# Optimization experiments

Measured on AMD Instinct MI355X. Metric: run time of the kernel, lower is better.

## Reference

```python
import jax, jax.numpy as jnp
import numpy as np
import math

M = 8                      # multiplicity (channels per irrep)
COMBOS = [(0,0,0),(0,1,1),(1,0,1),(1,1,0),(1,1,1),(2,1,1)]  # (edge_l, node_l, out_l)

def _cg_coeff(j1, m1, j2, m2, j3, m3):
    # standard (Racah) complex Clebsch-Gordan coefficient <j1 m1 j2 m2 | j3 m3>
    if m3 != m1 + m2:
        return 0.0
    f = math.factorial
    vmin = max(0, j2 - j3 - m1, j1 + m2 - j3)
    vmax = min(j1 + j2 - j3, j1 - m1, j2 + m2)
    pref = (2*j3 + 1) * f(j3+j1-j2) * f(j3-j1+j2) * f(j1+j2-j3) / f(j1+j2+j3+1)
    pref *= f(j3+m3) * f(j3-m3) * f(j1-m1) * f(j1+m1) * f(j2-m2) * f(j2+m2)
    s = 0.0
    for v in range(vmin, vmax + 1):
        s += (-1)**v / (f(v) * f(j1+j2-j3-v) * f(j1-m1-v) * f(j2+m2-v)
                        * f(j3-j2+m1+v) * f(j3-j1-m2+v))
    return math.sqrt(pref) * s

def _su2_cg(l1, l2, l3):
    C = np.zeros((2*l1+1, 2*l2+1, 2*l3+1), dtype=np.complex128)
    for m1 in range(-l1, l1+1):
        for m2 in range(-l2, l2+1):
            m3 = m1 + m2
            if -l3 <= m3 <= l3:
                C[m1+l1, m2+l2, m3+l3] = _cg_coeff(l1, m1, l2, m2, l3, m3)
    return C

def _qmat(l):
    # real -> complex spherical-harmonic change of basis (e3nn convention)
    q = np.zeros((2*l+1, 2*l+1), dtype=np.complex128)
    for m in range(-l, 0):
        q[l+m, l+abs(m)] = 1/np.sqrt(2)
        q[l+m, l-abs(m)] = -1j/np.sqrt(2)
    q[l, l] = 1.0
    for m in range(1, l+1):
        q[l+m, l+abs(m)] = (-1)**m / np.sqrt(2)
        q[l+m, l-abs(m)] = 1j * (-1)**m / np.sqrt(2)
    return (-1j)**l * q

def _so3_cg(l1, l2, l3):
    # real-basis CG, normalized to unit Frobenius norm (matches e3nn _so3_clebsch_gordan)
    C = np.einsum('ij,kl,mn,ikn->jlm', _qmat(l1), _qmat(l2),
                  np.conj(_qmat(l3)).T, _su2_cg(l1, l2, l3))
    assert np.abs(C.imag).max() < 1e-6
    C = C.real
    return C / np.linalg.norm(C)

CG = {c: jnp.asarray(_so3_cg(*c), dtype=jnp.float32) for c in COMBOS}


def setup_inputs() -> dict:
    N, E = 100000, 1600000
    ks = jax.random.split(jax.random.key(0), 6)
    return {
        'node_irreps': jax.random.normal(ks[0], (N, 4*M), jnp.float32),
        'edge_index': jax.random.randint(ks[1], (2, E), 0, N, dtype=jnp.int32),
        'sh0': jax.random.normal(ks[2], (E, 1), jnp.float32),
        'sh1': jax.random.normal(ks[3], (E, 3), jnp.float32),
        'sh2': jax.random.normal(ks[4], (E, 5), jnp.float32),
        'W': jax.random.normal(ks[5], (len(COMBOS), M, M), jnp.float32),
    }


def reference(node_irreps, edge_index, sh0, sh1, sh2, W):
    N, E = node_irreps.shape[0], edge_index.shape[1]
    src = node_irreps[edge_index[0]]                    # gather: [E, 4M]
    feats = {0: src[:, :M][:, :, None],                 # scalar channels [E, M, 1]
             1: src[:, M:].reshape(E, M, 3)}            # vector channels [E, M, 3]
    sh = {0: sh0, 1: sh1, 2: sh2}
    msg = {0: jnp.zeros((E, M, 1), node_irreps.dtype),
           1: jnp.zeros((E, M, 3), node_irreps.dtype)}
    for idx, (le, ln, lo) in enumerate(COMBOS):
        # per-edge CG tensor product: [de,dn,do] x [E,de] x [E,M,dn] -> [E,M,do]
        base = jnp.einsum('ijk,ei,emj->emk', CG[(le, ln, lo)], sh[le], feats[ln])
        # channel-mixing scalar weights (in_channel -> out_channel)
        msg[lo] = msg[lo] + jnp.einsum('io,eik->eok', W[idx], base)
    tgt = edge_index[1]
    agg0 = jax.ops.segment_sum(msg[0].reshape(E, M), tgt, num_segments=N)     # [N, M]
    agg1 = jax.ops.segment_sum(msg[1].reshape(E, 3*M), tgt, num_segments=N)   # [N, 3M]
    return jnp.concatenate([agg0, agg1], axis=1)
```

## Files before the change

### kernel.cpp

```cpp
#include <hip/hip_runtime.h>

#define THREADS 256

typedef float v4f __attribute__((ext_vector_type(4)));


__global__ __launch_bounds__(THREADS) void k_hist2(const int* __restrict__ tgt,
                                                   int* __restrict__ cnt,
                                                   int* __restrict__ ke, int E) {
    int e = blockIdx.x * THREADS + threadIdx.x;
    if (e < E) ke[e] = atomicAdd(&cnt[tgt[e]], 1);
}

__global__ __launch_bounds__(THREADS) void k_hist(const int* __restrict__ tgt,
                                                  int* __restrict__ cnt, int E) {
    int e = blockIdx.x * THREADS + threadIdx.x;
    if (e < E) atomicAdd(&cnt[tgt[e]], 1);
}

__global__ __launch_bounds__(THREADS) void k_scan_partial(const int* __restrict__ cnt,
                                                          int* __restrict__ bsum, int N) {
    __shared__ int lds[THREADS];
    int base = blockIdx.x * 1024 + threadIdx.x * 4;
    int s = 0;
    #pragma unroll
    for (int k = 0; k < 4; ++k) { int i = base + k; if (i < N) s += cnt[i]; }
    lds[threadIdx.x] = s; __syncthreads();
    for (int off = THREADS / 2; off > 0; off >>= 1) {
        if (threadIdx.x < off) lds[threadIdx.x] += lds[threadIdx.x + off];
        __syncthreads();
    }
    if (threadIdx.x == 0) bsum[blockIdx.x] = lds[0];
}

__global__ __launch_bounds__(THREADS) void k_scan_final2(int* __restrict__ cnt,
                                                         const int* __restrict__ bsum,
                                                         int* __restrict__ rowptr,
                                                         int N, int E, int NB) {
    __shared__ int lbs[THREADS];
    __shared__ int lds[THREADS];
    const int t = threadIdx.x;

    lbs[t] = (t < NB) ? bsum[t] : 0;
    __syncthreads();
    for (int off = 1; off < THREADS; off <<= 1) {
        int x = (t >= off) ? lbs[t - off] : 0;
        __syncthreads();
        lbs[t] += x;
        __syncthreads();
    }
    const int chunkBase = (blockIdx.x > 0) ? lbs[blockIdx.x - 1] : 0;

    int base = blockIdx.x * 1024 + t * 4;
    int v[4]; int local = 0;
    #pragma unroll
    for (int k = 0; k < 4; ++k) {
        int i = base + k;
        v[k] = (i < N) ? cnt[i] : 0;
        local += v[k];
    }
    lds[t] = local; __syncthreads();
    for (int off = 1; off < THREADS; off <<= 1) {
        int x = (t >= off) ? lds[t - off] : 0;
        __syncthreads();
        lds[t] += x;
        __syncthreads();
    }
    int p = lds[t] - local + chunkBase;
    #pragma unroll
    for (int k = 0; k < 4; ++k) {
        int i = base + k;
        if (i < N) { rowptr[i] = p; cnt[i] = p; p += v[k]; }
    }
    if (blockIdx.x == 0 && t == 0) rowptr[N] = E;
}


__global__ __launch_bounds__(THREADS) void k_scatter5(const int* __restrict__ eidx,
                                                      const int* __restrict__ ke,
                                                      const int* __restrict__ rowptr,
                                                      int* __restrict__ cursor,
                                                      const float* __restrict__ sh0,
                                                      const float* __restrict__ sh1,
                                                      const float* __restrict__ sh2,
                                                      float* __restrict__ pay,
                                                      int E) {
    int e = blockIdx.x * THREADS + threadIdx.x;
    if (e >= E) return;

    constexpr float IS10 = 0.31622776601683794f;
    constexpr float IS30 = 0.18257418583505536f;

    const int src = eidx[e];
    const int tgt = eidx[E + e];
    int pos;
    if (ke) pos = rowptr[tgt] + ke[e];
    else    pos = atomicAdd(&cursor[tgt], 1);

    const float s  = __builtin_nontemporal_load(&sh0[e]);
    const float u0 = __builtin_nontemporal_load(&sh1[3*e+0]);
    const float u1 = __builtin_nontemporal_load(&sh1[3*e+1]);
    const float u2 = __builtin_nontemporal_load(&sh1[3*e+2]);
    const float q0 = __builtin_nontemporal_load(&sh2[5*e+0]);
    const float q1 = __builtin_nontemporal_load(&sh2[5*e+1]);
    const float q2 = __builtin_nontemporal_load(&sh2[5*e+2]);
    const float q3 = __builtin_nontemporal_load(&sh2[5*e+3]);
    const float q4 = __builtin_nontemporal_load(&sh2[5*e+4]);

    const float Q00 = -q2*IS30 - q4*IS10;
    const float Q01 =  q1*IS10;
    const float Q02 =  q0*IS10;
    const float Q11 =  2.0f*q2*IS30;
    const float Q12 =  q3*IS10;
    const float Q22 = -q2*IS30 + q4*IS10;

    float4* pr = (float4*)(pay + (size_t)pos * 16);
    pr[0] = make_float4(s, u0, u1, u2);
    pr[1] = make_float4(Q00, Q01, Q02, Q11);
    pr[2] = make_float4(Q12, Q22, __int_as_float(src), 0.f);
    pr[3] = make_float4(0.f, 0.f, 0.f, 0.f);
}


#define ACC_STRIDE 15

__global__ __launch_bounds__(THREADS) void k_agg8(const float* __restrict__ node,
                                                  const int*   __restrict__ rowptr,
                                                  const float* __restrict__ pay,
                                                  const float* __restrict__ W,
                                                  float*       __restrict__ out,
                                                  int N) {
    __shared__ float sW[384];
    __shared__ float sAcc[32 * 8 * ACC_STRIDE];
    for (int t = threadIdx.x; t < 384; t += THREADS) sW[t] = W[t];
    __syncthreads();

    constexpr float IS3 = 0.57735026918962576f;
    constexpr float IS6 = 0.40824829046386302f;

    const int lane  = threadIdx.x & 63;
    const int wv    = threadIdx.x >> 6;
    const int i     = lane & 7;
    const int jslot = lane >> 3;

    for (int t = 0; t < 8; ++t) {
        const int n = blockIdx.x * 32 + wv * 8 + t;

        float a[14];
        #pragma unroll
        for (int k = 0; k < 14; ++k) a[k] = 0.f;

        if (n < N) {
            const int jbeg = rowptr[n];
            const int jend = rowptr[n + 1];

            if (jbeg < jend) {
                int j  = jbeg + jslot;
                int jc = (j < jend) ? j : (jend - 1);
                float mcur = (j < jend) ? 1.f : 0.f;
                const v4f* p = (const v4f*)(pay + (size_t)jc * 16);
                v4f c0 = p[0], c1 = p[1], c2 = p[2];
                int src = __float_as_int(c2[2]);
                const float* nr = node + (size_t)src * 32;
                v4f nf;
                nf[0] = nr[i];
                nf[1] = nr[8 + 3*i + 0];
                nf[2] = nr[8 + 3*i + 1];
                nf[3] = nr[8 + 3*i + 2];

                for (int g0 = jbeg; g0 < jend; g0 += 8) {
                    const int gn = g0 + 8;
                    const bool more = gn < jend;
                    v4f d0, d1, d2; float mnext = 0.f;
                    if (more) {
                        int jn  = gn + jslot;
                        int jnc = (jn < jend) ? jn : (jend - 1);
                        mnext = (jn < jend) ? 1.f : 0.f;
                        const v4f* pn = (const v4f*)(pay + (size_t)jnc * 16);
                        d0 = pn[0]; d1 = pn[1]; d2 = pn[2];
                    }

                    const float f0 = nf[0] * mcur;
                    const float x  = nf[1] * mcur;
                    const float y  = nf[2] * mcur;
                    const float z  = nf[3] * mcur;
                    const float s   = c0[0], u0 = c0[1], u1 = c0[2], u2 = c0[3];
                    const float Q00 = c1[0], Q01 = c1[1], Q02 = c1[2], Q11 = c1[3];
                    const float Q12 = c2[0], Q22 = c2[1];

                    a[0]  += s * f0;
                    a[1]  += u0*x + u1*y + u2*z;
                    a[2]  += s * x;
                    a[3]  += s * y;
                    a[4]  += s * z;
                    a[5]  += f0 * u0;
                    a[6]  += f0 * u1;
                    a[7]  += f0 * u2;
                    a[8]  += u1*z - u2*y;
                    a[9]  += u2*x - u0*z;
                    a[10] += u0*y - u1*x;
                    a[11] += Q00*x + Q01*y + Q02*z;
                    a[12] += Q01*x + Q11*y + Q12*z;
                    a[13] += Q02*x + Q12*y + Q22*z;

                    if (more) {
                        int srcn = __float_as_int(d2[2]);
                        const float* nrn = node + (size_t)srcn * 32;
                        nf[0] = nrn[i];
                        nf[1] = nrn[8 + 3*i + 0];
                        nf[2] = nrn[8 + 3*i + 1];
                        nf[3] = nrn[8 + 3*i + 2];
                        c0 = d0; c1 = d1; c2 = d2; mcur = mnext;
                    }
                }
            }
        }

        #pragma unroll
        for (int k = 0; k < 14; ++k) {
            float v = a[k];
            v += __shfl_xor(v, 8);
            v += __shfl_xor(v, 16);
            v += __shfl_xor(v, 32);
            a[k] = v;
        }

        if (n < N && jslot == 0) {
            #pragma unroll
            for (int k = 1; k < 8; ++k) a[k] *= IS3;
            #pragma unroll
            for (int k = 8; k < 11; ++k) a[k] *= IS6;
            float* myAcc = &sAcc[((wv * 8 + t) * 8 + i) * ACC_STRIDE];
            #pragma unroll
            for (int k = 0; k < 14; ++k) myAcc[k] = a[k];
        }
    }
    __syncthreads();

    {
        const int nodeSlot = threadIdx.x >> 3;
        const int o        = threadIdx.x & 7;
        const int n        = blockIdx.x * 32 + nodeSlot;
        if (n < N) {
            float o0 = 0.f, ox = 0.f, oy = 0.f, oz = 0.f;
            #pragma unroll
            for (int ii = 0; ii < 8; ++ii) {
                const float* A = &sAcc[(nodeSlot * 8 + ii) * ACC_STRIDE];
                const float w0 = sW[  0 + ii*8 + o];
                const float w1 = sW[ 64 + ii*8 + o];
                const float w2 = sW[128 + ii*8 + o];
                const float w3 = sW[192 + ii*8 + o];
                const float w4 = sW[256 + ii*8 + o];
                const float w5 = sW[320 + ii*8 + o];
                o0 += w0*A[0]  + w3*A[1];
                ox += w1*A[2]  + w2*A[5] + w4*A[8]  + w5*A[11];
                oy += w1*A[3]  + w2*A[6] + w4*A[9]  + w5*A[12];
                oz += w1*A[4]  + w2*A[7] + w4*A[10] + w5*A[13];
            }
            float* orow = out + (size_t)n * 32;
            orow[o]         = o0;
            orow[8 + 3*o+0] = ox;
            orow[8 + 3*o+1] = oy;
            orow[8 + 3*o+2] = oz;
        }
    }
}


__global__ __launch_bounds__(THREADS) void msg_kernel_atomic(
    const float* __restrict__ node,
    const int*   __restrict__ eidx,
    const float* __restrict__ sh0,
    const float* __restrict__ sh1,
    const float* __restrict__ sh2,
    const float* __restrict__ W,
    float*       __restrict__ out,
    int E)
{
    __shared__ float sW[384];
    for (int t = threadIdx.x; t < 384; t += THREADS) sW[t] = W[t];
    __syncthreads();

    int e = blockIdx.x * THREADS + threadIdx.x;
    if (e >= E) return;

    constexpr float IS3  = 0.57735026918962576f;
    constexpr float IS6  = 0.40824829046386302f;
    constexpr float IS10 = 0.31622776601683794f;
    constexpr float IS30 = 0.18257418583505536f;

    const int src = eidx[e];
    const int tgt = eidx[E + e];

    const float s  = sh0[e];
    const float u0 = sh1[3*e+0], u1 = sh1[3*e+1], u2 = sh1[3*e+2];
    const float q0 = sh2[5*e+0], q1 = sh2[5*e+1], q2 = sh2[5*e+2],
                q3 = sh2[5*e+3], q4 = sh2[5*e+4];

    const float Q00 = -q2*IS30 - q4*IS10;
    const float Q01 =  q1*IS10;
    const float Q02 =  q0*IS10;
    const float Q11 =  2.0f*q2*IS30;
    const float Q12 =  q3*IS10;
    const float Q22 = -q2*IS30 + q4*IS10;

    float f[32];
    {
        const float4* nr = (const float4*)(node + (size_t)src * 32);
        #pragma unroll
        for (int i = 0; i < 8; ++i) {
            float4 v = nr[i];
            f[4*i+0]=v.x; f[4*i+1]=v.y; f[4*i+2]=v.z; f[4*i+3]=v.w;
        }
    }

    float msg[32];
    #pragma unroll
    for (int j = 0; j < 32; ++j) msg[j] = 0.0f;

    const float s13 = s * IS3;

    #pragma unroll
    for (int i = 0; i < 8; ++i) {
        const float f0i = f[i];
        const float x = f[8+3*i+0], y = f[8+3*i+1], z = f[8+3*i+2];
        const float c0  = s * f0i;
        const float c3  = IS3 * (u0*x + u1*y + u2*z);
        const float p2  = IS3 * f0i;
        const float c1x = s13*x, c1y = s13*y, c1z = s13*z;
        const float c2x = p2*u0, c2y = p2*u1, c2z = p2*u2;
        const float c4x = IS6*(u1*z - u2*y);
        const float c4y = IS6*(u2*x - u0*z);
        const float c4z = IS6*(u0*y - u1*x);
        const float c5x = Q00*x + Q01*y + Q02*z;
        const float c5y = Q01*x + Q11*y + Q12*z;
        const float c5z = Q02*x + Q12*y + Q22*z;

        float wr[6][8];
        #pragma unroll
        for (int c = 0; c < 6; ++c) {
            float4 aa = *(const float4*)&sW[c*64 + i*8 + 0];
            float4 bb = *(const float4*)&sW[c*64 + i*8 + 4];
            wr[c][0]=aa.x; wr[c][1]=aa.y; wr[c][2]=aa.z; wr[c][3]=aa.w;
            wr[c][4]=bb.x; wr[c][5]=bb.y; wr[c][6]=bb.z; wr[c][7]=bb.w;
        }

        #pragma unroll
        for (int o = 0; o < 8; ++o) {
            msg[o] += wr[0][o]*c0 + wr[3][o]*c3;
            msg[8+3*o+0] += wr[1][o]*c1x + wr[2][o]*c2x + wr[4][o]*c4x + wr[5][o]*c5x;
            msg[8+3*o+1] += wr[1][o]*c1y + wr[2][o]*c2y + wr[4][o]*c4y + wr[5][o]*c5y;
            msg[8+3*o+2] += wr[1][o]*c1z + wr[2][o]*c2z + wr[4][o]*c4z + wr[5][o]*c5z;
        }
    }

    float* orow = out + (size_t)tgt * 32;
    #pragma unroll
    for (int j = 0; j < 32; ++j) unsafeAtomicAdd(orow + j, msg[j]);
}


extern "C" void kernel_launch(void* const* d_in, const int* in_sizes, int n_in,
                              void* d_out, int out_size, void* d_ws, size_t ws_size,
                              hipStream_t stream) {
    const float* node = (const float*)d_in[0];
    const int*   eidx = (const int*)d_in[1];
    const float* sh0  = (const float*)d_in[2];
    const float* sh1  = (const float*)d_in[3];
    const float* sh2  = (const float*)d_in[4];
    const float* W    = (const float*)d_in[5];
    float* out = (float*)d_out;

    const int E = in_sizes[2];
    const int N = in_sizes[0] / 32;
    const int NB = (N + 1023) / 1024;

    size_t base_w = (size_t)N + (size_t)(N + 1) + 256;
    size_t intA_w = base_w + (size_t)E;
    size_t payA   = (intA_w + 15) & ~(size_t)15;
    size_t payB   = (base_w + 15) & ~(size_t)15;
    size_t needA  = (payA + (size_t)E * 16) * sizeof(float);
    size_t needB  = (payB + (size_t)E * 16) * sizeof(float);

    const int gridE = (E + THREADS - 1) / THREADS;

    if (ws_size >= needB && NB <= THREADS) {
        const bool useKe = (ws_size >= needA);

        int* wsI    = (int*)d_ws;
        int* cnt    = wsI;
        int* rowptr = cnt + N;
        int* bsum   = rowptr + (N + 1);
        int* ke     = useKe ? (bsum + 256) : nullptr;
        float* pay  = (float*)d_ws + (useKe ? payA : payB);

        hipMemsetAsync(cnt, 0, (size_t)N * sizeof(int), stream);

        if (useKe)
            k_hist2<<<gridE, THREADS, 0, stream>>>(eidx + E, cnt, ke, E);
        else
            k_hist<<<gridE, THREADS, 0, stream>>>(eidx + E, cnt, E);

        k_scan_partial<<<NB, THREADS, 0, stream>>>(cnt, bsum, N);
        k_scan_final2<<<NB, THREADS, 0, stream>>>(cnt, bsum, rowptr, N, E, NB);

        k_scatter5<<<gridE, THREADS, 0, stream>>>(eidx, ke, rowptr, cnt,
                                                  sh0, sh1, sh2, pay, E);

        k_agg8<<<(N + 31) / 32, THREADS, 0, stream>>>(node, rowptr, pay, W, out, N);
    } else {
        hipMemsetAsync(d_out, 0, (size_t)out_size * sizeof(float), stream);
        msg_kernel_atomic<<<gridE, THREADS, 0, stream>>>(
            node, eidx, sh0, sh1, sh2, W, out, E);
    }
}
```

Before: 359.4 us.

## Scatter only edge/src index pairs and gather spherical harmonics in aggregation

Instead of scattering a 64-byte per-edge payload (precomputed SH and quadrupole terms plus src) into CSR order, the scatter kernel now writes only an 8-byte (edge id, src) pair. The aggregation kernel reads sh0/sh1/sh2 directly by edge id and recomputes the quadrupole matrix entries, with a two-level prefetch of the index pairs. This greatly reduces scatter write traffic and payload reads, but turns the SH reads in aggregation into random, uncoalesced gathers of 9 floats per edge.

```diff
diff --git a/kernel.cpp b/kernel.cpp
--- a/kernel.cpp
+++ b/kernel.cpp
@@ -3,6 +3,7 @@
 #define THREADS 256
 
 typedef float v4f __attribute__((ext_vector_type(4)));
+typedef int   v2i __attribute__((ext_vector_type(2)));
 
 
 __global__ __launch_bounds__(THREADS) void k_hist2(const int* __restrict__ tgt,
@@ -76,57 +77,32 @@
 }
 
 
-__global__ __launch_bounds__(THREADS) void k_scatter5(const int* __restrict__ eidx,
+__global__ __launch_bounds__(THREADS) void k_colscat2(const int* __restrict__ eidx,
                                                       const int* __restrict__ ke,
                                                       const int* __restrict__ rowptr,
                                                       int* __restrict__ cursor,
-                                                      const float* __restrict__ sh0,
-                                                      const float* __restrict__ sh1,
-                                                      const float* __restrict__ sh2,
-                                                      float* __restrict__ pay,
+                                                      int* __restrict__ col2,
                                                       int E) {
     int e = blockIdx.x * THREADS + threadIdx.x;
     if (e >= E) return;
-
-    constexpr float IS10 = 0.31622776601683794f;
-    constexpr float IS30 = 0.18257418583505536f;
-
     const int src = eidx[e];
     const int tgt = eidx[E + e];
     int pos;
     if (ke) pos = rowptr[tgt] + ke[e];
     else    pos = atomicAdd(&cursor[tgt], 1);
-
-    const float s  = __builtin_nontemporal_load(&sh0[e]);
-    const float u0 = __builtin_nontemporal_load(&sh1[3*e+0]);
-    const float u1 = __builtin_nontemporal_load(&sh1[3*e+1]);
-    const float u2 = __builtin_nontemporal_load(&sh1[3*e+2]);
-    const float q0 = __builtin_nontemporal_load(&sh2[5*e+0]);
-    const float q1 = __builtin_nontemporal_load(&sh2[5*e+1]);
-    const float q2 = __builtin_nontemporal_load(&sh2[5*e+2]);
-    const float q3 = __builtin_nontemporal_load(&sh2[5*e+3]);
-    const float q4 = __builtin_nontemporal_load(&sh2[5*e+4]);
-
-    const float Q00 = -q2*IS30 - q4*IS10;
-    const float Q01 =  q1*IS10;
-    const float Q02 =  q0*IS10;
-    const float Q11 =  2.0f*q2*IS30;
-    const float Q12 =  q3*IS10;
-    const float Q22 = -q2*IS30 + q4*IS10;
-
-    float4* pr = (float4*)(pay + (size_t)pos * 16);
-    pr[0] = make_float4(s, u0, u1, u2);
-    pr[1] = make_float4(Q00, Q01, Q02, Q11);
-    pr[2] = make_float4(Q12, Q22, __int_as_float(src), 0.f);
-    pr[3] = make_float4(0.f, 0.f, 0.f, 0.f);
+    v2i v; v[0] = e; v[1] = src;
+    *(v2i*)(col2 + 2*(size_t)pos) = v;
 }
 
 
 #define ACC_STRIDE 15
 
-__global__ __launch_bounds__(THREADS) void k_agg8(const float* __restrict__ node,
+__global__ __launch_bounds__(THREADS) void k_agg9(const float* __restrict__ node,
                                                   const int*   __restrict__ rowptr,
-                                                  const float* __restrict__ pay,
+                                                  const int*   __restrict__ col2,
+                                                  const float* __restrict__ sh0,
+                                                  const float* __restrict__ sh1,
+                                                  const float* __restrict__ sh2,
                                                   const float* __restrict__ W,
                                                   float*       __restrict__ out,
                                                   int N) {
@@ -135,8 +111,10 @@
     for (int t = threadIdx.x; t < 384; t += THREADS) sW[t] = W[t];
     __syncthreads();
 
-    constexpr float IS3 = 0.57735026918962576f;
-    constexpr float IS6 = 0.40824829046386302f;
+    constexpr float IS3  = 0.57735026918962576f;
+    constexpr float IS6  = 0.40824829046386302f;
+    constexpr float IS10 = 0.31622776601683794f;
+    constexpr float IS30 = 0.18257418583505536f;
 
     const int lane  = threadIdx.x & 63;
     const int wv    = threadIdx.x >> 6;
@@ -155,62 +133,83 @@
             const int jend = rowptr[n + 1];
 
             if (jbeg < jend) {
-                int j  = jbeg + jslot;
-                int jc = (j < jend) ? j : (jend - 1);
-                float mcur = (j < jend) ? 1.f : 0.f;
-                const v4f* p = (const v4f*)(pay + (size_t)jc * 16);
-                v4f c0 = p[0], c1 = p[1], c2 = p[2];
-                int src = __float_as_int(c2[2]);
-                const float* nr = node + (size_t)src * 32;
-                v4f nf;
-                nf[0] = nr[i];
-                nf[1] = nr[8 + 3*i + 0];
-                nf[2] = nr[8 + 3*i + 1];
-                nf[3] = nr[8 + 3*i + 2];
+                const int jlast = jend - 1;
+
+                int j0  = jbeg + jslot;
+                int jc0 = (j0 < jend) ? j0 : jlast;
+                float mcur = (j0 < jend) ? 1.f : 0.f;
+                v2i ec = *(const v2i*)(col2 + 2*(size_t)jc0);
+                float s  = sh0[ec[0]];
+                const float* up = sh1 + 3*(size_t)ec[0];
+                float u0 = up[0], u1 = up[1], u2 = up[2];
+                const float* qp = sh2 + 5*(size_t)ec[0];
+                float q0 = qp[0], q1 = qp[1], q2 = qp[2], q3 = qp[3], q4 = qp[4];
+                const float* nr = node + (size_t)ec[1] * 32;
+                float f0 = nr[i];
+                float x  = nr[8 + 3*i + 0];
+                float y  = nr[8 + 3*i + 1];
+                float z  = nr[8 + 3*i + 2];
+                int j1  = jbeg + 8 + jslot;
+                int jc1 = (j1 < jend) ? j1 : jlast;
+                v2i ecn = *(const v2i*)(col2 + 2*(size_t)jc1);
 
                 for (int g0 = jbeg; g0 < jend; g0 += 8) {
                     const int gn = g0 + 8;
                     const bool more = gn < jend;
-                    v4f d0, d1, d2; float mnext = 0.f;
+                    float ns = 0.f, nu0 = 0.f, nu1 = 0.f, nu2 = 0.f;
+                    float nq0 = 0.f, nq1 = 0.f, nq2 = 0.f, nq3 = 0.f, nq4 = 0.f;
+                    float nf0 = 0.f, nx = 0.f, ny = 0.f, nz = 0.f;
+                    float mnext = 0.f;
+                    v2i ec2 = ecn;
                     if (more) {
-                        int jn  = gn + jslot;
-                        int jnc = (jn < jend) ? jn : (jend - 1);
-                        mnext = (jn < jend) ? 1.f : 0.f;
-                        const v4f* pn = (const v4f*)(pay + (size_t)jnc * 16);
-                        d0 = pn[0]; d1 = pn[1]; d2 = pn[2];
+                        mnext = (gn + jslot < jend) ? 1.f : 0.f;
+                        ns = sh0[ecn[0]];
+                        const float* nup = sh1 + 3*(size_t)ecn[0];
+                        nu0 = nup[0]; nu1 = nup[1]; nu2 = nup[2];
+                        const float* nqp = sh2 + 5*(size_t)ecn[0];
+                        nq0 = nqp[0]; nq1 = nqp[1]; nq2 = nqp[2]; nq3 = nqp[3]; nq4 = nqp[4];
+                        const float* nrn = node + (size_t)ecn[1] * 32;
+                        nf0 = nrn[i];
+                        nx  = nrn[8 + 3*i + 0];
+                        ny  = nrn[8 + 3*i + 1];
+                        nz  = nrn[8 + 3*i + 2];
+                        int j2  = gn + 8 + jslot;
+                        int jc2 = (j2 < jend) ? j2 : jlast;
+                        ec2 = *(const v2i*)(col2 + 2*(size_t)jc2);
                     }
 
-                    const float f0 = nf[0] * mcur;
-                    const float x  = nf[1] * mcur;
-                    const float y  = nf[2] * mcur;
-                    const float z  = nf[3] * mcur;
-                    const float s   = c0[0], u0 = c0[1], u1 = c0[2], u2 = c0[3];
-                    const float Q00 = c1[0], Q01 = c1[1], Q02 = c1[2], Q11 = c1[3];
-                    const float Q12 = c2[0], Q22 = c2[1];
-
-                    a[0]  += s * f0;
-                    a[1]  += u0*x + u1*y + u2*z;
-                    a[2]  += s * x;
-                    a[3]  += s * y;
-                    a[4]  += s * z;
-                    a[5]  += f0 * u0;
-                    a[6]  += f0 * u1;
-                    a[7]  += f0 * u2;
-                    a[8]  += u1*z - u2*y;
-                    a[9]  += u2*x - u0*z;
-                    a[10] += u0*y - u1*x;
-                    a[11] += Q00*x + Q01*y + Q02*z;
-                    a[12] += Q01*x + Q11*y + Q12*z;
-                    a[13] += Q02*x + Q12*y + Q22*z;
+                    const float mf0 = f0 * mcur;
+                    const float mx  = x  * mcur;
+                    const float my  = y  * mcur;
+                    const float mz  = z  * mcur;
+
+                    const float Q00 = -q2*IS30 - q4*IS10;
+                    const float Q01 =  q1*IS10;
+                    const float Q02 =  q0*IS10;
+                    const float Q11 =  2.0f*q2*IS30;
+                    const float Q12 =  q3*IS10;
+                    const float Q22 = -q2*IS30 + q4*IS10;
+
+                    a[0]  += s * mf0;
+                    a[1]  += u0*mx + u1*my + u2*mz;
+                    a[2]  += s * mx;
+                    a[3]  += s * my;
+                    a[4]  += s * mz;
+                    a[5]  += mf0 * u0;
+                    a[6]  += mf0 * u1;
+                    a[7]  += mf0 * u2;
+                    a[8]  += u1*mz - u2*my;
+                    a[9]  += u2*mx - u0*mz;
+                    a[10] += u0*my - u1*mx;
+                    a[11] += Q00*mx + Q01*my + Q02*mz;
+                    a[12] += Q01*mx + Q11*my + Q12*mz;
+                    a[13] += Q02*mx + Q12*my + Q22*mz;
 
                     if (more) {
-                        int srcn = __float_as_int(d2[2]);
-                        const float* nrn = node + (size_t)srcn * 32;
-                        nf[0] = nrn[i];
-                        nf[1] = nrn[8 + 3*i + 0];
-                        nf[2] = nrn[8 + 3*i + 1];
-                        nf[3] = nrn[8 + 3*i + 2];
-                        c0 = d0; c1 = d1; c2 = d2; mcur = mnext;
+                        s = ns; u0 = nu0; u1 = nu1; u2 = nu2;
+                        q0 = nq0; q1 = nq1; q2 = nq2; q3 = nq3; q4 = nq4;
+                        f0 = nf0; x = nx; y = ny; z = nz;
+                        ecn = ec2; mcur = mnext;
                     }
                 }
             }
@@ -377,10 +376,10 @@
 
     size_t base_w = (size_t)N + (size_t)(N + 1) + 256;
     size_t intA_w = base_w + (size_t)E;
-    size_t payA   = (intA_w + 15) & ~(size_t)15;
-    size_t payB   = (base_w + 15) & ~(size_t)15;
-    size_t needA  = (payA + (size_t)E * 16) * sizeof(float);
-    size_t needB  = (payB + (size_t)E * 16) * sizeof(float);
+    size_t colA   = (intA_w + 3) & ~(size_t)3;
+    size_t colB   = (base_w + 3) & ~(size_t)3;
+    size_t needA  = (colA + 2*(size_t)E) * sizeof(float);
+    size_t needB  = (colB + 2*(size_t)E) * sizeof(float);
 
     const int gridE = (E + THREADS - 1) / THREADS;
 
@@ -392,7 +391,7 @@
         int* rowptr = cnt + N;
         int* bsum   = rowptr + (N + 1);
         int* ke     = useKe ? (bsum + 256) : nullptr;
-        float* pay  = (float*)d_ws + (useKe ? payA : payB);
+        int* col2   = wsI + (useKe ? colA : colB);
 
         hipMemsetAsync(cnt, 0, (size_t)N * sizeof(int), stream);
 
@@ -404,10 +403,10 @@
         k_scan_partial<<<NB, THREADS, 0, stream>>>(cnt, bsum, N);
         k_scan_final2<<<NB, THREADS, 0, stream>>>(cnt, bsum, rowptr, N, E, NB);
 
-        k_scatter5<<<gridE, THREADS, 0, stream>>>(eidx, ke, rowptr, cnt,
-                                                  sh0, sh1, sh2, pay, E);
-
-        k_agg8<<<(N + 31) / 32, THREADS, 0, stream>>>(node, rowptr, pay, W, out, N);
+        k_colscat2<<<gridE, THREADS, 0, stream>>>(eidx, ke, rowptr, cnt, col2, E);
+
+        k_agg9<<<(N + 31) / 32, THREADS, 0, stream>>>(node, rowptr, col2,
+                                                      sh0, sh1, sh2, W, out, N);
     } else {
         hipMemsetAsync(d_out, 0, (size_t)out_size * sizeof(float), stream);
         msg_kernel_atomic<<<gridE, THREADS, 0, stream>>>(
```

Result: faster. 337.1 us (-6.2%).
